# Optimization experiments

Measured on AMD Instinct MI355X. Metric: run time of the kernel, lower is better.

## Reference

```python
import jax, jax.numpy as jnp
import numpy as np

D_MODEL = 1024
NUM_HEADS = 16
D_HEAD = D_MODEL // NUM_HEADS
ROPE_THETA = 10000.0


def _rope(x, pos):
    # x: [..., S, d_head]; rotate consecutive pairs (2i, 2i+1)
    half = x.shape[-1] // 2
    inv_freq = ROPE_THETA ** (-jnp.arange(half, dtype=jnp.float32) * 2.0 / x.shape[-1])
    ang = pos[:, None].astype(jnp.float32) * inv_freq[None, :]  # [S, half]
    cos, sin = jnp.cos(ang), jnp.sin(ang)
    x1, x2 = x[..., 0::2], x[..., 1::2]
    r1 = x1 * cos - x2 * sin
    r2 = x1 * sin + x2 * cos
    return jnp.stack([r1, r2], axis=-1).reshape(x.shape)


def setup_inputs() -> dict:
    key = jax.random.key(0)
    ks = jax.random.split(key, 5)
    s = 1.0 / np.sqrt(D_MODEL)
    return {
        "q_weight": jax.random.normal(ks[0], (D_MODEL, D_MODEL), jnp.float32) * s,
        "k_weight": jax.random.normal(ks[1], (D_MODEL, D_MODEL), jnp.float32) * s,
        "v_weight": jax.random.normal(ks[2], (D_MODEL, D_MODEL), jnp.float32) * s,
        "o_weight": jax.random.normal(ks[3], (D_MODEL, D_MODEL), jnp.float32) * s,
        "in_features": jax.random.normal(ks[4], (2, 2048, D_MODEL), jnp.float32),
    }


def reference(q_weight, k_weight, v_weight, o_weight, in_features):
    S = in_features.shape[-2]
    qw = q_weight.reshape(NUM_HEADS, D_HEAD, D_MODEL)
    kw = k_weight.reshape(NUM_HEADS, D_HEAD, D_MODEL)
    vw = v_weight.reshape(NUM_HEADS, D_HEAD, D_MODEL)
    # [B, H, S, d_head]
    q = jnp.einsum('bsj,nhj->bnsh', in_features, qw)
    k = jnp.einsum('bsj,nhj->bnsh', in_features, kw)
    v = jnp.einsum('bsj,nhj->bnsh', in_features, vw)
    pos = jnp.arange(S)
    q = _rope(q, pos)
    k = _rope(k, pos)
    scale = 1.0 / jnp.sqrt(jnp.asarray(D_HEAD, dtype=q.dtype))
    scores = jnp.einsum('bnqh,bnkh->bnqk', q, k) * scale  # [B,H,S,S]
    causal = jnp.tril(jnp.ones((S, S), dtype=bool))
    scores = jnp.where(causal, scores, jnp.asarray(-jnp.inf, dtype=scores.dtype))
    attn = jax.nn.softmax(scores, axis=-1)
    out = jnp.einsum('bnqk,bnkh->bnqh', attn, v)  # [B,H,S,d_head]
    out = jnp.swapaxes(out, -2, -3).reshape(*out.shape[:-3], S, D_MODEL)
    return jnp.einsum('ji,bki->bkj', o_weight, out)
```

## Files before the change

### kernel.cpp

```cpp
#include <hip/hip_runtime.h>
#include <math.h>

typedef __attribute__((ext_vector_type(8))) short bf16x8;
typedef __attribute__((ext_vector_type(4))) short bf16x4;
typedef __attribute__((ext_vector_type(4))) float f32x4;
typedef __attribute__((ext_vector_type(2))) unsigned int u32x2;

static constexpr int D_MODEL = 1024;
static constexpr int SEQ = 2048;
static constexpr int BATCH = 2;
static constexpr int M_TOT = BATCH * SEQ;

__device__ __forceinline__ unsigned short f2bf(float f) {
  unsigned int u = __builtin_bit_cast(unsigned int, f);
  u += 0x7fffu + ((u >> 16) & 1u);
  return (unsigned short)(u >> 16);
}

__device__ __forceinline__ unsigned int cvtpk(float lo, float hi) {
  unsigned int r;
  asm volatile("v_cvt_pk_bf16_f32 %0, %1, %2" : "=v"(r) : "v"(lo), "v"(hi));
  return r;
}

__device__ __forceinline__ void gld16(const unsigned short* g, unsigned short* l) {
  __builtin_amdgcn_global_load_lds(
      (const __attribute__((address_space(1))) unsigned int*)g,
      (__attribute__((address_space(3))) unsigned int*)l, 16, 0, 0);
}

__global__ void cvt_f32_bf16(const float* __restrict__ src,
                             unsigned short* __restrict__ dst, int n4) {
  int i = blockIdx.x * blockDim.x + threadIdx.x;
  if (i >= n4) return;
  const float4 v = reinterpret_cast<const float4*>(src)[i];
  ushort4 o;
  o.x = f2bf(v.x); o.y = f2bf(v.y); o.z = f2bf(v.z); o.w = f2bf(v.w);
  reinterpret_cast<ushort4*>(dst)[i] = o;
}

__global__ void cvt_weights(const float* __restrict__ qw, const float* __restrict__ kw,
                            const float* __restrict__ vw, const float* __restrict__ ow,
                            unsigned short* __restrict__ dst) {
  int i = blockIdx.x * blockDim.x + threadIdx.x;
  const int which = i >> 18;
  const int off = i & 262143;
  const float* src = (which == 0) ? qw : (which == 1) ? kw : (which == 2) ? vw : ow;
  const float4 v = reinterpret_cast<const float4*>(src)[off];
  ushort4 o;
  o.x = f2bf(v.x); o.y = f2bf(v.y); o.z = f2bf(v.z); o.w = f2bf(v.w);
  reinterpret_cast<ushort4*>(dst)[i] = o;
}

__global__ void rope_tables(float2* __restrict__ ct2) {
  int idx = blockIdx.x * blockDim.x + threadIdx.x;
  int s = idx >> 5;
  int p = idx & 31;
  float inv_freq = powf(10000.0f, -(float)p / 32.0f);
  float ang = (float)s * inv_freq;
  int psw = p ^ (((s >> 2) & 1) << 3);
  float2 cs; cs.x = cosf(ang); cs.y = sinf(ang);
  ct2[s * 32 + psw] = cs;
}

template <int BM, int BN, int MODE>
__global__ __launch_bounds__(256, 2)
void gemm2(const unsigned short* __restrict__ A,
           const unsigned short* __restrict__ W,
           unsigned short* __restrict__ Qd,
           unsigned short* __restrict__ Kd,
           unsigned short* __restrict__ Vd,
           float* __restrict__ Fd,
           const float2* __restrict__ ct2) {
  constexpr int MI = BM / 32, NI = BN / 32;
  constexpr int NKT = D_MODEL / 32;
  constexpr int LOADS = BM / 64 + BN / 64;
  __shared__ __align__(16) unsigned short smem[2 * (BM + BN) * 32];
  unsigned short* Asm = smem;
  unsigned short* Bsm = smem + 2 * BM * 32;
  const int tid  = threadIdx.x;
  const int lane = tid & 63;
  const int wave = tid >> 6;
  const int wm = wave >> 1, wn = wave & 1;
  const int m0 = blockIdx.y * BM;
  const int n0 = blockIdx.x * BN;
  const int lr = lane & 15, lg = lane >> 4;

  const int srow = lane >> 2;
  const int scol = ((lane & 3) ^ ((lane >> 3) & 3)) * 8;

  auto stage = [&](int buf, int kt) {
    const int k0 = kt * 32;
#pragma unroll
    for (int rr = 0; rr < BM / 64; ++rr) {
      const int ch = rr * 4 + wave;
      gld16(&A[(size_t)(m0 + ch * 16 + srow) * D_MODEL + k0 + scol], &Asm[buf * BM * 32 + ch * 512]);
    }
#pragma unroll
    for (int rr = 0; rr < BN / 64; ++rr) {
      const int ch = rr * 4 + wave;
      gld16(&W[(size_t)(n0 + ch * 16 + srow) * D_MODEL + k0 + scol], &Bsm[buf * BN * 32 + ch * 512]);
    }
  };

  f32x4 acc[MI][NI] = {};

  stage(0, 0);
  stage(1, 1);
  __builtin_amdgcn_sched_barrier(0);

  const int swz = (lg ^ ((lr >> 1) & 3)) * 8;

  for (int kt = 0; kt < NKT; ++kt) {
    const int cur = kt & 1;
    if (kt + 1 < NKT) {
      if constexpr (LOADS == 4) asm volatile("s_waitcnt vmcnt(4)" ::: "memory");
      else                      asm volatile("s_waitcnt vmcnt(3)" ::: "memory");
    } else {
      asm volatile("s_waitcnt vmcnt(0)" ::: "memory");
    }
    __builtin_amdgcn_s_barrier();
    __builtin_amdgcn_sched_barrier(0);

    bf16x8 af[MI], bfr[NI];
#pragma unroll
    for (int i = 0; i < MI; ++i)
      af[i] = *reinterpret_cast<const bf16x8*>(&Asm[cur * BM * 32 + (wm * (BM / 2) + i * 16 + lr) * 32 + swz]);
#pragma unroll
    for (int j = 0; j < NI; ++j)
      bfr[j] = *reinterpret_cast<const bf16x8*>(&Bsm[cur * BN * 32 + (wn * (BN / 2) + j * 16 + lr) * 32 + swz]);
    asm volatile("s_waitcnt lgkmcnt(0)" ::: "memory");
    __builtin_amdgcn_sched_barrier(0);
    __builtin_amdgcn_s_barrier();
    __builtin_amdgcn_sched_barrier(0);

    if (kt + 2 < NKT) stage(cur, kt + 2);
    __builtin_amdgcn_sched_barrier(0);

#pragma unroll
    for (int i = 0; i < MI; ++i)
#pragma unroll
      for (int j = 0; j < NI; ++j)
        acc[i][j] = __builtin_amdgcn_mfma_f32_16x16x32_bf16(af[i], bfr[j], acc[i][j], 0, 0, 0);
  }

  if constexpr (MODE == 2) {
#pragma unroll
    for (int i = 0; i < MI; ++i)
#pragma unroll
      for (int j = 0; j < NI; ++j)
#pragma unroll
        for (int r = 0; r < 4; ++r) {
          const int gm = m0 + wm * (BM / 2) + i * 16 + lg * 4 + r;
          const int gc = n0 + wn * (BN / 2) + j * 16 + lr;
          Fd[(size_t)gm * D_MODEL + gc] = acc[i][j][r];
        }
  } else {
    const int t = n0 >> 10;
    const int b = m0 >> 11;
    const int s_base = m0 & 2047;
    if (t < 2) {
      unsigned short* dstQ = (t == 0) ? Qd : Kd;
      const unsigned short* gsrc = (const unsigned short*)(ct2 + (size_t)s_base * 32);
#pragma unroll
      for (int it = 0; it < 8; ++it) {
        const int ch = wave * 8 + it;
        gld16(&gsrc[ch * 512 + lane * 8], &smem[ch * 512]);
      }
      asm volatile("s_waitcnt vmcnt(0)" ::: "memory");
      __builtin_amdgcn_sched_barrier(0);
      __builtin_amdgcn_s_barrier();
      const float2* tbl = (const float2*)smem;
      const int nbase = (n0 & 1023) >> 6;
#pragma unroll
      for (int i = 0; i < MI; ++i) {
#pragma unroll
        for (int j = 0; j < NI; ++j) {
#pragma unroll
          for (int r = 0; r < 4; ++r) {
            const int sl = wm * (BM / 2) + i * 16 + lg * 4 + r;
            const int h  = j * 16 + lr;
            const int psw = (h >> 1) ^ (((sl >> 2) & 1) << 3);
            const float2 cs = tbl[sl * 32 + psw];
            float x = acc[i][j][r];
            const float part = __shfl_xor(x, 1, 64);
            x = (h & 1) ? (part * cs.y + x * cs.x) : (x * cs.x - part * cs.y);
            const int n = nbase + wn;
            dstQ[(size_t)((b * 16 + n) * SEQ + s_base + sl) * 64 + h] = f2bf(x);
          }
        }
      }
    } else {
      unsigned short* tile = smem;
      const int row = tid >> 2;
      const int ck  = tid & 3;
      for (int pass = 0; pass < 2; ++pass) {
        __builtin_amdgcn_s_barrier();
        if (wn == pass) {
#pragma unroll
          for (int i = 0; i < MI; ++i)
#pragma unroll
            for (int j = 0; j < NI; ++j)
#pragma unroll
              for (int r = 0; r < 4; ++r)
                tile[(j * 16 + lr) * 136 + wm * 64 + i * 16 + lg * 4 + r] = f2bf(acc[i][j][r]);
        }
        asm volatile("s_waitcnt lgkmcnt(0)" ::: "memory");
        __builtin_amdgcn_sched_barrier(0);
        __builtin_amdgcn_s_barrier();
        const int c = (n0 & 1023) + pass * 64 + row;
        const int n = c >> 6, h = c & 63;
        unsigned short* vrow = &Vd[(size_t)((b * 16 + n) * 64 + h) * SEQ + s_base + ck * 32];
        const unsigned short* lrow = &tile[row * 136 + ck * 32];
#pragma unroll
        for (int k = 0; k < 4; ++k)
          *reinterpret_cast<bf16x8*>(&vrow[k * 8]) = *reinterpret_cast<const bf16x8*>(&lrow[k * 8]);
      }
    }
  }
}

__global__ __launch_bounds__(256, 2)
void attn_kernel(const unsigned short* __restrict__ Q,
                 const unsigned short* __restrict__ K,
                 const unsigned short* __restrict__ Vt,
                 unsigned short* __restrict__ AO) {
  __shared__ __align__(16) unsigned short Ksh[2][4096];
  __shared__ __align__(16) unsigned short Vsh[2][4096];
  const int bn   = blockIdx.x;
  const int j    = (gridDim.y - 1) - blockIdx.y;
  const int wave = threadIdx.x >> 6;
  const int lane = threadIdx.x & 63;
  const int lr = lane & 15, lg = lane >> 4;
  const int q0 = j * 128 + wave * 32;
  const unsigned short* Qh = Q  + (size_t)bn * SEQ * 64;
  const unsigned short* Kh = K  + (size_t)bn * SEQ * 64;
  const unsigned short* Vh = Vt + (size_t)bn * 64 * SEQ;
  const int b = bn >> 4, n = bn & 15;

  const int srow8 = lane >> 3;
  const int scolb = ((lane & 7) ^ srow8) * 8;

  auto stage = [&](int buf, int k0) {
#pragma unroll
    for (int c = 0; c < 2; ++c) {
      const int ch = wave * 2 + c;
      const int row = ch * 8 + srow8;
      gld16(&Kh[(size_t)(k0 + row) * 64 + scolb], &Ksh[buf][ch * 512]);
      gld16(&Vh[(size_t)row * SEQ + k0 + scolb], &Vsh[buf][ch * 512]);
    }
  };

  constexpr float KL2E = 0.125f * 1.44269504088896f;
  const int nt = 2 * j + 2;

  bf16x8 qf[2][2];
#pragma unroll
  for (int mi = 0; mi < 2; ++mi)
#pragma unroll
    for (int ks = 0; ks < 2; ++ks)
      qf[mi][ks] = *reinterpret_cast<const bf16x8*>(
          &Qh[(size_t)(q0 + mi * 16 + lr) * 64 + ks * 32 + lg * 8]);
  asm volatile("s_waitcnt vmcnt(0)" ::: "memory");
  __builtin_amdgcn_sched_barrier(0);

  f32x4 o[2][4] = {};
  float ls[2] = {0.f, 0.f};

  stage(0, 0);
  stage(1, 64);
  __builtin_amdgcn_sched_barrier(0);

  for (int t = 0; t < nt; ++t) {
    const int cur = t & 1;
    const int k0 = t * 64;
    if (t + 1 < nt) { asm volatile("s_waitcnt vmcnt(4)" ::: "memory"); }
    else            { asm volatile("s_waitcnt vmcnt(0)" ::: "memory"); }
    __builtin_amdgcn_s_barrier();
    __builtin_amdgcn_sched_barrier(0);

    const unsigned short* Kc = &Ksh[cur][0];
    const unsigned short* Vc = &Vsh[cur][0];

    bf16x8 kf[4][2];
#pragma unroll
    for (int nj = 0; nj < 4; ++nj)
#pragma unroll
      for (int ks = 0; ks < 2; ++ks) {
        const int R = nj * 16 + lr;
        const int p = (ks * 4 + lg) ^ (R & 7);
        kf[nj][ks] = *reinterpret_cast<const bf16x8*>(&Kc[R * 64 + p * 8]);
      }
    f32x4 sf[2][4] = {};
    __builtin_amdgcn_s_setprio(1);
#pragma unroll
    for (int nj = 0; nj < 4; ++nj)
#pragma unroll
      for (int ks = 0; ks < 2; ++ks)
#pragma unroll
        for (int mi = 0; mi < 2; ++mi)
          sf[mi][nj] = __builtin_amdgcn_mfma_f32_16x16x32_bf16(kf[nj][ks], qf[mi][ks], sf[mi][nj], 0, 0, 0);
    __builtin_amdgcn_s_setprio(0);

    bf16x4 vB[4][4];
#pragma unroll
    for (int nj = 0; nj < 4; ++nj)
#pragma unroll
      for (int hf = 0; hf < 4; ++hf) {
        const int R = hf * 16 + lr;
        const int c = nj * 2 + (lg >> 1);
        const int p = ((c ^ (R & 7)) << 3) + (lg & 1) * 4;
        vB[nj][hf] = *reinterpret_cast<const bf16x4*>(&Vc[R * 64 + p]);
      }

    u32x2 w[2][4];
    if (k0 + 63 <= q0) {
#pragma unroll
      for (int mi = 0; mi < 2; ++mi)
#pragma unroll
        for (int nj = 0; nj < 4; ++nj) {
          const float p0 = __builtin_amdgcn_exp2f(sf[mi][nj][0] * KL2E);
          const float p1 = __builtin_amdgcn_exp2f(sf[mi][nj][1] * KL2E);
          const float p2 = __builtin_amdgcn_exp2f(sf[mi][nj][2] * KL2E);
          const float p3 = __builtin_amdgcn_exp2f(sf[mi][nj][3] * KL2E);
          ls[mi] += (p0 + p1) + (p2 + p3);
          w[mi][nj][0] = cvtpk(p0, p1);
          w[mi][nj][1] = cvtpk(p2, p3);
        }
    } else {
#pragma unroll
      for (int mi = 0; mi < 2; ++mi) {
        const int qrow = q0 + mi * 16 + lr;
#pragma unroll
        for (int nj = 0; nj < 4; ++nj) {
          const int kb = k0 + nj * 16 + lg * 4;
          float p[4];
#pragma unroll
          for (int r = 0; r < 4; ++r)
            p[r] = (kb + r <= qrow) ? __builtin_amdgcn_exp2f(sf[mi][nj][r] * KL2E) : 0.0f;
          ls[mi] += (p[0] + p[1]) + (p[2] + p[3]);
          w[mi][nj][0] = cvtpk(p[0], p[1]);
          w[mi][nj][1] = cvtpk(p[2], p[3]);
        }
      }
    }

    asm volatile("s_waitcnt lgkmcnt(0)" ::: "memory");
    __builtin_amdgcn_sched_barrier(0);
    __builtin_amdgcn_s_barrier();
    __builtin_amdgcn_sched_barrier(0);

    if (t + 2 < nt) stage(cur, (t + 2) * 64);
    __builtin_amdgcn_sched_barrier(0);

    __builtin_amdgcn_s_setprio(1);
#pragma unroll
    for (int nj = 0; nj < 4; ++nj)
#pragma unroll
      for (int hf = 0; hf < 4; ++hf)
#pragma unroll
        for (int mi = 0; mi < 2; ++mi)
          o[mi][hf] = __builtin_amdgcn_mfma_f32_16x16x16bf16_1k(
              __builtin_bit_cast(bf16x4, w[mi][nj]), vB[nj][hf], o[mi][hf], 0, 0, 0);
    __builtin_amdgcn_s_setprio(0);
  }

#pragma unroll
  for (int mi = 0; mi < 2; ++mi) {
    float s = ls[mi];
    s += __shfl_xor(s, 16, 64);
    s += __shfl_xor(s, 32, 64);
    ls[mi] = s;
  }
#pragma unroll
  for (int mi = 0; mi < 2; ++mi)
#pragma unroll
    for (int r = 0; r < 4; ++r) {
      const float sv = __shfl(ls[mi], lg * 4 + r, 64);
      const float inv = 1.0f / sv;
      const int srow = q0 + mi * 16 + lg * 4 + r;
#pragma unroll
      for (int hf = 0; hf < 4; ++hf) {
        const int h = hf * 16 + lr;
        AO[(size_t)(b * SEQ + srow) * D_MODEL + n * 64 + h] = f2bf(o[mi][hf][r] * inv);
      }
    }
}

extern "C" void kernel_launch(void* const* d_in, const int* in_sizes, int n_in,
                              void* d_out, int out_size, void* d_ws, size_t ws_size,
                              hipStream_t stream) {
  const float* qw = (const float*)d_in[0];
  const float* kw = (const float*)d_in[1];
  const float* vw = (const float*)d_in[2];
  const float* ow = (const float*)d_in[3];
  const float* x  = (const float*)d_in[4];

  char* ws = (char*)d_ws;
  const size_t XB = (size_t)M_TOT * D_MODEL * 2;
  const size_t WB = (size_t)D_MODEL * D_MODEL * 2;
  unsigned short* Xb  = (unsigned short*)ws;  ws += XB;
  unsigned short* Wqb = (unsigned short*)ws;  ws += WB;
  unsigned short* Wkb = (unsigned short*)ws;  ws += WB;
  unsigned short* Wvb = (unsigned short*)ws;  ws += WB;
  unsigned short* Wob = (unsigned short*)ws;  ws += WB;
  unsigned short* Qr  = (unsigned short*)ws;  ws += XB;
  unsigned short* Kr  = (unsigned short*)ws;  ws += XB;
  unsigned short* Vt  = (unsigned short*)ws;  ws += XB;
  unsigned short* AO  = (unsigned short*)ws;  ws += XB;
  float2* ct2 = (float2*)ws;  ws += (size_t)SEQ * 32 * 8;
  (void)Wkb; (void)Wvb;

  cvt_f32_bf16<<<(M_TOT * D_MODEL / 4) / 256, 256, 0, stream>>>(x, Xb, M_TOT * D_MODEL / 4);
  cvt_weights<<<(4 * D_MODEL * D_MODEL / 4) / 256, 256, 0, stream>>>(qw, kw, vw, ow, Wqb);
  rope_tables<<<(SEQ * 32) / 256, 256, 0, stream>>>(ct2);

  gemm2<128, 128, 0><<<dim3(3072 / 128, M_TOT / 128), 256, 0, stream>>>(
      Xb, Wqb, Qr, Kr, Vt, nullptr, ct2);

  attn_kernel<<<dim3(BATCH * 16, 16), 256, 0, stream>>>(Qr, Kr, Vt, AO);

  gemm2<128, 64, 2><<<dim3(D_MODEL / 64, M_TOT / 128), 256, 0, stream>>>(
      AO, Wob, nullptr, nullptr, nullptr, (float*)d_out, nullptr);
}
```

Before: 105.5 us.

## Double the attention KV tile to 128 keys per barrier stage

The K/V tile staged into LDS per iteration grows from 64 to 128 keys, which halves the number of loop iterations and barriers. Each iteration runs two 64-key halves in sequence. The V LDS swizzle changes to a 16-way XOR for the wider 128-column rows. The PV MFMAs now run before the end-of-iteration barrier, so the next-stage prefetch is issued after all compute instead of overlapping with the PV matmul. LDS use doubles to 64KB per block, which may reduce how many blocks can be resident per CU.

```diff
diff --git a/kernel.cpp b/kernel.cpp
--- a/kernel.cpp
+++ b/kernel.cpp
@@ -225,8 +225,8 @@
                  const unsigned short* __restrict__ K,
                  const unsigned short* __restrict__ Vt,
                  unsigned short* __restrict__ AO) {
-  __shared__ __align__(16) unsigned short Ksh[2][4096];
-  __shared__ __align__(16) unsigned short Vsh[2][4096];
+  __shared__ __align__(16) unsigned short Ksh[2][8192];
+  __shared__ __align__(16) unsigned short Vsh[2][8192];
   const int bn   = blockIdx.x;
   const int j    = (gridDim.y - 1) - blockIdx.y;
   const int wave = threadIdx.x >> 6;
@@ -238,21 +238,23 @@
   const unsigned short* Vh = Vt + (size_t)bn * 64 * SEQ;
   const int b = bn >> 4, n = bn & 15;
 
-  const int srow8 = lane >> 3;
-  const int scolb = ((lane & 7) ^ srow8) * 8;
-
   auto stage = [&](int buf, int k0) {
 #pragma unroll
-    for (int c = 0; c < 2; ++c) {
-      const int ch = wave * 2 + c;
-      const int row = ch * 8 + srow8;
-      gld16(&Kh[(size_t)(k0 + row) * 64 + scolb], &Ksh[buf][ch * 512]);
-      gld16(&Vh[(size_t)row * SEQ + k0 + scolb], &Vsh[buf][ch * 512]);
+    for (int c = 0; c < 4; ++c) {
+      const int ch = wave * 4 + c;
+      const int row = ch * 8 + (lane >> 3);
+      gld16(&Kh[(size_t)(k0 + row) * 64 + ((lane & 7) ^ (row & 7)) * 8], &Ksh[buf][ch * 512]);
+    }
+#pragma unroll
+    for (int c = 0; c < 4; ++c) {
+      const int ch = wave * 4 + c;
+      const int row = ch * 4 + (lane >> 4);
+      gld16(&Vh[(size_t)row * SEQ + k0 + ((lane & 15) ^ (row & 15)) * 8], &Vsh[buf][ch * 512]);
     }
   };
 
   constexpr float KL2E = 0.125f * 1.44269504088896f;
-  const int nt = 2 * j + 2;
+  const int nt = j + 1;
 
   bf16x8 qf[2][2];
 #pragma unroll
@@ -268,13 +270,12 @@
   float ls[2] = {0.f, 0.f};
 
   stage(0, 0);
-  stage(1, 64);
+  stage(1, 128);
   __builtin_amdgcn_sched_barrier(0);
 
   for (int t = 0; t < nt; ++t) {
     const int cur = t & 1;
-    const int k0 = t * 64;
-    if (t + 1 < nt) { asm volatile("s_waitcnt vmcnt(4)" ::: "memory"); }
+    if (t + 1 < nt) { asm volatile("s_waitcnt vmcnt(8)" ::: "memory"); }
     else            { asm volatile("s_waitcnt vmcnt(0)" ::: "memory"); }
     __builtin_amdgcn_s_barrier();
     __builtin_amdgcn_sched_barrier(0);
@@ -282,67 +283,83 @@
     const unsigned short* Kc = &Ksh[cur][0];
     const unsigned short* Vc = &Vsh[cur][0];
 
-    bf16x8 kf[4][2];
-#pragma unroll
-    for (int nj = 0; nj < 4; ++nj)
-#pragma unroll
-      for (int ks = 0; ks < 2; ++ks) {
-        const int R = nj * 16 + lr;
-        const int p = (ks * 4 + lg) ^ (R & 7);
-        kf[nj][ks] = *reinterpret_cast<const bf16x8*>(&Kc[R * 64 + p * 8]);
+#pragma unroll
+    for (int kh = 0; kh < 2; ++kh) {
+      const int k0h = t * 128 + kh * 64;
+
+      bf16x8 kf[4][2];
+#pragma unroll
+      for (int nj = 0; nj < 4; ++nj)
+#pragma unroll
+        for (int ks = 0; ks < 2; ++ks) {
+          const int R = kh * 64 + nj * 16 + lr;
+          const int p = (ks * 4 + lg) ^ (R & 7);
+          kf[nj][ks] = *reinterpret_cast<const bf16x8*>(&Kc[R * 64 + p * 8]);
+        }
+      f32x4 sf[2][4] = {};
+      __builtin_amdgcn_s_setprio(1);
+#pragma unroll
+      for (int nj = 0; nj < 4; ++nj)
+#pragma unroll
+        for (int ks = 0; ks < 2; ++ks)
+#pragma unroll
+          for (int mi = 0; mi < 2; ++mi)
+            sf[mi][nj] = __builtin_amdgcn_mfma_f32_16x16x32_bf16(kf[nj][ks], qf[mi][ks], sf[mi][nj], 0, 0, 0);
+      __builtin_amdgcn_s_setprio(0);
+
+      bf16x4 vB[4][4];
+#pragma unroll
+      for (int nj = 0; nj < 4; ++nj)
+#pragma unroll
+        for (int hf = 0; hf < 4; ++hf) {
+          const int R = hf * 16 + lr;
+          const int c0 = kh * 8 + nj * 2 + (lg >> 1);
+          const int p = ((c0 ^ (R & 15)) << 3) + (lg & 1) * 4;
+          vB[nj][hf] = *reinterpret_cast<const bf16x4*>(&Vc[R * 128 + p]);
+        }
+
+      u32x2 w[2][4];
+      if (k0h + 63 <= q0) {
+#pragma unroll
+        for (int mi = 0; mi < 2; ++mi)
+#pragma unroll
+          for (int nj = 0; nj < 4; ++nj) {
+            const float p0 = __builtin_amdgcn_exp2f(sf[mi][nj][0] * KL2E);
+            const float p1 = __builtin_amdgcn_exp2f(sf[mi][nj][1] * KL2E);
+            const float p2 = __builtin_amdgcn_exp2f(sf[mi][nj][2] * KL2E);
+            const float p3 = __builtin_amdgcn_exp2f(sf[mi][nj][3] * KL2E);
+            ls[mi] += (p0 + p1) + (p2 + p3);
+            w[mi][nj][0] = cvtpk(p0, p1);
+            w[mi][nj][1] = cvtpk(p2, p3);
+          }
+      } else {
+#pragma unroll
+        for (int mi = 0; mi < 2; ++mi) {
+          const int qrow = q0 + mi * 16 + lr;
+#pragma unroll
+          for (int nj = 0; nj < 4; ++nj) {
+            const int kb = k0h + nj * 16 + lg * 4;
+            float p[4];
+#pragma unroll
+            for (int r = 0; r < 4; ++r)
+              p[r] = (kb + r <= qrow) ? __builtin_amdgcn_exp2f(sf[mi][nj][r] * KL2E) : 0.0f;
+            ls[mi] += (p[0] + p[1]) + (p[2] + p[3]);
+            w[mi][nj][0] = cvtpk(p[0], p[1]);
+            w[mi][nj][1] = cvtpk(p[2], p[3]);
+          }
+        }
       }
-    f32x4 sf[2][4] = {};
-    __builtin_amdgcn_s_setprio(1);
-#pragma unroll
-    for (int nj = 0; nj < 4; ++nj)
-#pragma unroll
-      for (int ks = 0; ks < 2; ++ks)
-#pragma unroll
-        for (int mi = 0; mi < 2; ++mi)
-          sf[mi][nj] = __builtin_amdgcn_mfma_f32_16x16x32_bf16(kf[nj][ks], qf[mi][ks], sf[mi][nj], 0, 0, 0);
-    __builtin_amdgcn_s_setprio(0);
-
-    bf16x4 vB[4][4];
-#pragma unroll
-    for (int nj = 0; nj < 4; ++nj)
-#pragma unroll
-      for (int hf = 0; hf < 4; ++hf) {
-        const int R = hf * 16 + lr;
-        const int c = nj * 2 + (lg >> 1);
-        const int p = ((c ^ (R & 7)) << 3) + (lg & 1) * 4;
-        vB[nj][hf] = *reinterpret_cast<const bf16x4*>(&Vc[R * 64 + p]);
-      }
-
-    u32x2 w[2][4];
-    if (k0 + 63 <= q0) {
-#pragma unroll
-      for (int mi = 0; mi < 2; ++mi)
-#pragma unroll
-        for (int nj = 0; nj < 4; ++nj) {
-          const float p0 = __builtin_amdgcn_exp2f(sf[mi][nj][0] * KL2E);
-          const float p1 = __builtin_amdgcn_exp2f(sf[mi][nj][1] * KL2E);
-          const float p2 = __builtin_amdgcn_exp2f(sf[mi][nj][2] * KL2E);
-          const float p3 = __builtin_amdgcn_exp2f(sf[mi][nj][3] * KL2E);
-          ls[mi] += (p0 + p1) + (p2 + p3);
-          w[mi][nj][0] = cvtpk(p0, p1);
-          w[mi][nj][1] = cvtpk(p2, p3);
-        }
-    } else {
-#pragma unroll
-      for (int mi = 0; mi < 2; ++mi) {
-        const int qrow = q0 + mi * 16 + lr;
-#pragma unroll
-        for (int nj = 0; nj < 4; ++nj) {
-          const int kb = k0 + nj * 16 + lg * 4;
-          float p[4];
-#pragma unroll
-          for (int r = 0; r < 4; ++r)
-            p[r] = (kb + r <= qrow) ? __builtin_amdgcn_exp2f(sf[mi][nj][r] * KL2E) : 0.0f;
-          ls[mi] += (p[0] + p[1]) + (p[2] + p[3]);
-          w[mi][nj][0] = cvtpk(p[0], p[1]);
-          w[mi][nj][1] = cvtpk(p[2], p[3]);
-        }
-      }
+
+      __builtin_amdgcn_s_setprio(1);
+#pragma unroll
+      for (int nj = 0; nj < 4; ++nj)
+#pragma unroll
+        for (int hf = 0; hf < 4; ++hf)
+#pragma unroll
+          for (int mi = 0; mi < 2; ++mi)
+            o[mi][hf] = __builtin_amdgcn_mfma_f32_16x16x16bf16_1k(
+                __builtin_bit_cast(bf16x4, w[mi][nj]), vB[nj][hf], o[mi][hf], 0, 0, 0);
+      __builtin_amdgcn_s_setprio(0);
     }
 
     asm volatile("s_waitcnt lgkmcnt(0)" ::: "memory");
@@ -350,19 +367,8 @@
     __builtin_amdgcn_s_barrier();
     __builtin_amdgcn_sched_barrier(0);
 
-    if (t + 2 < nt) stage(cur, (t + 2) * 64);
-    __builtin_amdgcn_sched_barrier(0);
-
-    __builtin_amdgcn_s_setprio(1);
-#pragma unroll
-    for (int nj = 0; nj < 4; ++nj)
-#pragma unroll
-      for (int hf = 0; hf < 4; ++hf)
-#pragma unroll
-        for (int mi = 0; mi < 2; ++mi)
-          o[mi][hf] = __builtin_amdgcn_mfma_f32_16x16x16bf16_1k(
-              __builtin_bit_cast(bf16x4, w[mi][nj]), vB[nj][hf], o[mi][hf], 0, 0, 0);
-    __builtin_amdgcn_s_setprio(0);
+    if (t + 2 < nt) stage(cur, (t + 2) * 128);
+    __builtin_amdgcn_sched_barrier(0);
   }
 
 #pragma unroll
```

After: 106.3 us. Within noise of the previous version (+0.8%).

## Double GEMM K-tile depth to 64 and reorder attention query-block schedule

Applied to the files above, without the earlier changes.

Raises the GEMM's K step from 32 to 64 per pipeline stage, halving the number of loop iterations and barriers. It uses a new 8-way XOR swizzle for the 64-wide LDS rows and issues two MFMA k-substeps per stage. The price is twice the LDS and more registers for fragments, which may cut occupancy. Separately, the attention grid is remapped so the first eight y-blocks take the longest causal rows, followed by the shortest ones, to improve load balance.

```diff
diff --git a/kernel.cpp b/kernel.cpp
--- a/kernel.cpp
+++ b/kernel.cpp
@@ -73,11 +73,11 @@
            float* __restrict__ Fd,
            const float2* __restrict__ ct2) {
   constexpr int MI = BM / 32, NI = BN / 32;
-  constexpr int NKT = D_MODEL / 32;
-  constexpr int LOADS = BM / 64 + BN / 64;
-  __shared__ __align__(16) unsigned short smem[2 * (BM + BN) * 32];
+  constexpr int NKT = D_MODEL / 64;
+  constexpr int LOADS = BM / 32 + BN / 32;
+  __shared__ __align__(16) unsigned short smem[2 * (BM + BN) * 64];
   unsigned short* Asm = smem;
-  unsigned short* Bsm = smem + 2 * BM * 32;
+  unsigned short* Bsm = smem + 2 * BM * 64;
   const int tid  = threadIdx.x;
   const int lane = tid & 63;
   const int wave = tid >> 6;
@@ -86,20 +86,21 @@
   const int n0 = blockIdx.x * BN;
   const int lr = lane & 15, lg = lane >> 4;
 
-  const int srow = lane >> 2;
-  const int scol = ((lane & 3) ^ ((lane >> 3) & 3)) * 8;
-
   auto stage = [&](int buf, int kt) {
-    const int k0 = kt * 32;
-#pragma unroll
-    for (int rr = 0; rr < BM / 64; ++rr) {
-      const int ch = rr * 4 + wave;
-      gld16(&A[(size_t)(m0 + ch * 16 + srow) * D_MODEL + k0 + scol], &Asm[buf * BM * 32 + ch * 512]);
-    }
-#pragma unroll
-    for (int rr = 0; rr < BN / 64; ++rr) {
-      const int ch = rr * 4 + wave;
-      gld16(&W[(size_t)(n0 + ch * 16 + srow) * D_MODEL + k0 + scol], &Bsm[buf * BN * 32 + ch * 512]);
+    const int k0 = kt * 64;
+#pragma unroll
+    for (int c = 0; c < BM / 32; ++c) {
+      const int ch = c * 4 + wave;
+      const int row = ch * 8 + (lane >> 3);
+      gld16(&A[(size_t)(m0 + row) * D_MODEL + k0 + ((lane & 7) ^ (row & 7)) * 8],
+            &Asm[buf * BM * 64 + ch * 512]);
+    }
+#pragma unroll
+    for (int c = 0; c < BN / 32; ++c) {
+      const int ch = c * 4 + wave;
+      const int row = ch * 8 + (lane >> 3);
+      gld16(&W[(size_t)(n0 + row) * D_MODEL + k0 + ((lane & 7) ^ (row & 7)) * 8],
+            &Bsm[buf * BN * 64 + ch * 512]);
     }
   };
 
@@ -109,26 +110,34 @@
   stage(1, 1);
   __builtin_amdgcn_sched_barrier(0);
 
-  const int swz = (lg ^ ((lr >> 1) & 3)) * 8;
-
   for (int kt = 0; kt < NKT; ++kt) {
     const int cur = kt & 1;
     if (kt + 1 < NKT) {
-      if constexpr (LOADS == 4) asm volatile("s_waitcnt vmcnt(4)" ::: "memory");
-      else                      asm volatile("s_waitcnt vmcnt(3)" ::: "memory");
+      if constexpr (LOADS == 8) asm volatile("s_waitcnt vmcnt(8)" ::: "memory");
+      else                      asm volatile("s_waitcnt vmcnt(6)" ::: "memory");
     } else {
       asm volatile("s_waitcnt vmcnt(0)" ::: "memory");
     }
     __builtin_amdgcn_s_barrier();
     __builtin_amdgcn_sched_barrier(0);
 
-    bf16x8 af[MI], bfr[NI];
+    bf16x8 af[MI][2], bfr[NI][2];
 #pragma unroll
     for (int i = 0; i < MI; ++i)
-      af[i] = *reinterpret_cast<const bf16x8*>(&Asm[cur * BM * 32 + (wm * (BM / 2) + i * 16 + lr) * 32 + swz]);
+#pragma unroll
+      for (int ks = 0; ks < 2; ++ks) {
+        const int R = wm * (BM / 2) + i * 16 + lr;
+        const int p = (ks * 4 + lg) ^ (R & 7);
+        af[i][ks] = *reinterpret_cast<const bf16x8*>(&Asm[cur * BM * 64 + R * 64 + p * 8]);
+      }
 #pragma unroll
     for (int j = 0; j < NI; ++j)
-      bfr[j] = *reinterpret_cast<const bf16x8*>(&Bsm[cur * BN * 32 + (wn * (BN / 2) + j * 16 + lr) * 32 + swz]);
+#pragma unroll
+      for (int ks = 0; ks < 2; ++ks) {
+        const int R = wn * (BN / 2) + j * 16 + lr;
+        const int p = (ks * 4 + lg) ^ (R & 7);
+        bfr[j][ks] = *reinterpret_cast<const bf16x8*>(&Bsm[cur * BN * 64 + R * 64 + p * 8]);
+      }
     asm volatile("s_waitcnt lgkmcnt(0)" ::: "memory");
     __builtin_amdgcn_sched_barrier(0);
     __builtin_amdgcn_s_barrier();
@@ -138,10 +147,12 @@
     __builtin_amdgcn_sched_barrier(0);
 
 #pragma unroll
-    for (int i = 0; i < MI; ++i)
-#pragma unroll
-      for (int j = 0; j < NI; ++j)
-        acc[i][j] = __builtin_amdgcn_mfma_f32_16x16x32_bf16(af[i], bfr[j], acc[i][j], 0, 0, 0);
+    for (int ks = 0; ks < 2; ++ks)
+#pragma unroll
+      for (int i = 0; i < MI; ++i)
+#pragma unroll
+        for (int j = 0; j < NI; ++j)
+          acc[i][j] = __builtin_amdgcn_mfma_f32_16x16x32_bf16(af[i][ks], bfr[j][ks], acc[i][j], 0, 0, 0);
   }
 
   if constexpr (MODE == 2) {
@@ -228,7 +239,8 @@
   __shared__ __align__(16) unsigned short Ksh[2][4096];
   __shared__ __align__(16) unsigned short Vsh[2][4096];
   const int bn   = blockIdx.x;
-  const int j    = (gridDim.y - 1) - blockIdx.y;
+  const int y    = blockIdx.y;
+  const int j    = (y < 8) ? (15 - y) : (y - 8);
   const int wave = threadIdx.x >> 6;
   const int lane = threadIdx.x & 63;
   const int lr = lane & 15, lg = lane >> 4;
```

New measurement: 102.1 us. 1.03x faster.
